# Kernel tuning notes

Measured on AMD Instinct MI355X. Metric: run time of the kernel, lower is better.

The kernel has to match this reference:

```python
import jax, jax.numpy as jnp
import numpy as np

N_NODES = 100000
N_EDGES = 3200000
D_FEAT = 64


def setup_inputs() -> dict:
    key = jax.random.key(0)
    k_x, k_r, k_c, k_v = jax.random.split(key, 4)
    x = jax.random.normal(k_x, (N_NODES, D_FEAT), dtype=jnp.float32)
    edge_row = jax.random.randint(k_r, (N_EDGES,), 0, N_NODES, dtype=jnp.int64)
    edge_col = jax.random.randint(k_c, (N_EDGES,), 0, N_NODES, dtype=jnp.int64)
    # positive values mimicking symmetric-normalized adjacency weights
    edge_val = jax.random.uniform(k_v, (N_EDGES,), dtype=jnp.float32)
    t = jnp.zeros((1,), dtype=jnp.float32)  # ODE time, unused by this linear GCN step
    return {"t": t, "x": x, "edge_row": edge_row, "edge_col": edge_col, "edge_val": edge_val}


def reference(t, x, edge_row, edge_col, edge_val):
    # out = A_sparse @ x, COO SpMM as gather -> scale -> segment-sum scatter
    # gathered: [n_edges, d]
    gathered = edge_val[:, None] * x[edge_col]
    out = jax.ops.segment_sum(gathered, edge_row, num_segments=N_NODES)
    return out
```

## Files before the change

kernel.cpp:

```cpp
#include <hip/hip_runtime.h>
#include <hip/hip_bf16.h>
#include <hip/hip_fp16.h>

#define D 64
#define RB 128
#define NB_MAX 1024
#define NBLK1 512
#define P1CAP 6272
#define CAP 5120

typedef unsigned long long ull;
typedef unsigned short u16;

__device__ __forceinline__ ull pack_rec(float v, int r, int c) {
    return ((ull)__float_as_uint(v) << 32) |
           (ull)(((unsigned)(r & (RB - 1)) << 17) | (unsigned)c);
}

__global__ __launch_bounds__(256) void spmm_atomic_kernel(
    const float* __restrict__ x,
    const int*   __restrict__ edge_row,
    const int*   __restrict__ edge_col,
    const float* __restrict__ edge_val,
    float*       __restrict__ out,
    int n_edges)
{
    const int gtid = blockIdx.x * blockDim.x + threadIdx.x;
    const int wave = gtid >> 6;
    const int lane = threadIdx.x & 63;
    if (wave >= n_edges) return;
    const int   r = edge_row[wave];
    const int   c = edge_col[wave];
    const float v = edge_val[wave];
    atomicAdd(&out[(size_t)r * D + lane], v * x[(size_t)c * D + lane]);
}

__global__ __launch_bounds__(256) void p1a_hist_kernel(
    const int* __restrict__ rows, u16* __restrict__ counts,
    int n_edges, int nb, int chunk)
{
    __shared__ int cnt[NB_MAX];
    const int t = threadIdx.x, blk = blockIdx.x;
    const int e0 = blk * chunk;
    const int e1 = min(e0 + chunk, n_edges);

    for (int i = t; i < nb; i += 256) cnt[i] = 0;
    __syncthreads();
    for (int i = e0 + t * 4; i < e1; i += 1024) {
        if (i + 4 <= e1) {
            const int4 r4 = *(const int4*)(rows + i);
            atomicAdd(&cnt[r4.x >> 7], 1);
            atomicAdd(&cnt[r4.y >> 7], 1);
            atomicAdd(&cnt[r4.z >> 7], 1);
            atomicAdd(&cnt[r4.w >> 7], 1);
        } else {
            for (int k = i; k < e1; ++k) atomicAdd(&cnt[rows[k] >> 7], 1);
        }
    }
    __syncthreads();
    for (int i = t; i < nb; i += 256)
        counts[(size_t)i * NBLK1 + blk] = (u16)cnt[i];
}

__global__ __launch_bounds__(256) void p2_scanblocks_kernel(
    const u16* __restrict__ counts, int* __restrict__ dest32,
    int* __restrict__ binsum, int nb)
{
    __shared__ int s[256];
    const int b = blockIdx.x, t = threadIdx.x;
    const int la = (int)counts[(size_t)b * NBLK1 + 2 * t];
    const int lb = (int)counts[(size_t)b * NBLK1 + 2 * t + 1];
    const int mysum = la + lb;
    s[t] = mysum;
    for (int off = 1; off < 256; off <<= 1) {
        __syncthreads();
        const int w = (t >= off) ? s[t - off] : 0;
        __syncthreads();
        s[t] += w;
    }
    const int excl = s[t] - mysum;
    dest32[(size_t)b * NBLK1 + 2 * t]     = excl;
    dest32[(size_t)b * NBLK1 + 2 * t + 1] = excl + la;
    if (t == 255) binsum[b] = s[255];
}

__global__ __launch_bounds__(1024) void p3_scanbins_kernel(
    const int* __restrict__ binsum, int* __restrict__ binbase,
    int* __restrict__ flags, int nb)
{
    __shared__ int s[1024];
    const int t = threadIdx.x;
    const int mine = (t < nb) ? binsum[t] : 0;
    s[t] = mine;
    for (int off = 1; off < 1024; off <<= 1) {
        __syncthreads();
        const int v = (t >= off) ? s[t - off] : 0;
        __syncthreads();
        s[t] += v;
    }
    if (t < nb) { binbase[t] = s[t] - mine; flags[t] = 0; }
    if (t == nb - 1) binbase[nb] = s[t];
}

__global__ __launch_bounds__(256) void p1b_sortwrite_kernel(
    const int* __restrict__ rows, const int* __restrict__ cols,
    const float* __restrict__ vals,
    const u16* __restrict__ counts, const int* __restrict__ dest32,
    const int* __restrict__ binbase,
    ull* __restrict__ recs, int n_edges, int nb, int chunk)
{
    __shared__ ull stage[P1CAP];
    __shared__ u16 binof[P1CAP];
    __shared__ int cnt[NB_MAX];
    __shared__ u16 doffL[NB_MAX];
    __shared__ int gbase[NB_MAX];
    __shared__ int s[256];
    const int t = threadIdx.x, blk = blockIdx.x;
    const int e0 = blk * chunk;
    const int e1 = min(e0 + chunk, n_edges);
    const int len = e1 - e0;

    int pre[4], sum = 0, c4[4];
    const int base = t * 4;
    #pragma unroll
    for (int k = 0; k < 4; ++k) {
        const int idx = base + k;
        c4[k] = (idx < nb) ? (int)counts[(size_t)idx * NBLK1 + blk] : 0;
        pre[k] = sum; sum += c4[k];
    }
    s[t] = sum;
    for (int off = 1; off < 256; off <<= 1) {
        __syncthreads();
        const int w = (t >= off) ? s[t - off] : 0;
        __syncthreads();
        s[t] += w;
    }
    const int texcl = s[t] - sum;
    __syncthreads();
    #pragma unroll
    for (int k = 0; k < 4; ++k) {
        const int idx = base + k;
        if (idx < nb) {
            const int e = texcl + pre[k];
            cnt[idx]   = e;
            doffL[idx] = (u16)e;
            gbase[idx] = binbase[idx] + dest32[(size_t)idx * NBLK1 + blk];
        }
    }
    __syncthreads();

    for (int i = e0 + t * 4; i < e1; i += 1024) {
        if (i + 4 <= e1) {
            const int4   r4  = *(const int4*)(rows + i);
            const int4   c4v = *(const int4*)(cols + i);
            const float4 v4  = *(const float4*)(vals + i);
            int p;
            p = atomicAdd(&cnt[r4.x >> 7], 1); stage[p] = pack_rec(v4.x, r4.x, c4v.x); binof[p] = (u16)(r4.x >> 7);
            p = atomicAdd(&cnt[r4.y >> 7], 1); stage[p] = pack_rec(v4.y, r4.y, c4v.y); binof[p] = (u16)(r4.y >> 7);
            p = atomicAdd(&cnt[r4.z >> 7], 1); stage[p] = pack_rec(v4.z, r4.z, c4v.z); binof[p] = (u16)(r4.z >> 7);
            p = atomicAdd(&cnt[r4.w >> 7], 1); stage[p] = pack_rec(v4.w, r4.w, c4v.w); binof[p] = (u16)(r4.w >> 7);
        } else {
            for (int k = i; k < e1; ++k) {
                const int p = atomicAdd(&cnt[rows[k] >> 7], 1);
                stage[p] = pack_rec(vals[k], rows[k], cols[k]);
                binof[p] = (u16)(rows[k] >> 7);
            }
        }
    }
    __syncthreads();

    for (int i = t; i < len; i += 256) {
        const int bin = (int)binof[i];
        recs[gbase[bin] + (i - (int)doffL[bin])] = stage[i];
    }
}

__global__ __launch_bounds__(256) void p4_sortbin_kernel(
    const int* __restrict__ binbase,
    ull* __restrict__ recs, int* __restrict__ offsets_row, int* __restrict__ flags,
    int n_nodes)
{
    __shared__ ull stage[CAP];
    __shared__ int cnt[1024];
    __shared__ int s[256];
    const int b = blockIdx.x, t = threadIdx.x;
    const int s0  = binbase[b];
    const int len = binbase[b + 1] - s0;

    if (len > CAP) {
        if (t == 0) {
            flags[b] = 1;
            if (b * RB <= n_nodes) offsets_row[b * RB] = s0;
        }
        return;
    }

    for (int i = t; i < 1024; i += 256) cnt[i] = 0;
    __syncthreads();

    for (int i = t; i < len; i += 256) {
        const ull rr = recs[s0 + i];
        stage[i] = rr;
        const int key = ((int)((rr >> 17) & (RB - 1)) << 3) |
                        (int)(((unsigned)rr & 0x1FFFF) >> 14);
        atomicAdd(&cnt[key], 1);
    }
    __syncthreads();

    int v[4], pre[4], sum = 0;
    const int base = t * 4;
    #pragma unroll
    for (int k = 0; k < 4; ++k) { v[k] = cnt[base + k]; pre[k] = sum; sum += v[k]; }
    s[t] = sum;
    for (int off = 1; off < 256; off <<= 1) {
        __syncthreads();
        const int w = (t >= off) ? s[t - off] : 0;
        __syncthreads();
        s[t] += w;
    }
    const int texcl = s[t] - sum;
    __syncthreads();
    #pragma unroll
    for (int k = 0; k < 4; ++k) cnt[base + k] = texcl + pre[k];
    __syncthreads();

    if (t <= RB) {
        const int r = b * RB + t;
        if (r <= n_nodes)
            offsets_row[r] = s0 + ((t == RB) ? len : cnt[t << 3]);
    }
    __syncthreads();

    for (int i = t; i < len; i += 256) {
        const ull rr = stage[i];
        const int key = ((int)((rr >> 17) & (RB - 1)) << 3) |
                        (int)(((unsigned)rr & 0x1FFFF) >> 14);
        const int p = atomicAdd(&cnt[key], 1);
        recs[s0 + p] = rr;
    }
}

__global__ void tohalf_kernel(const float* __restrict__ x,
                              __half2* __restrict__ xh2, int n4)
{
    for (int i = blockIdx.x * blockDim.x + threadIdx.x; i < n4;
         i += gridDim.x * blockDim.x) {
        const float4 v = ((const float4*)x)[i];
        xh2[2 * i + 0] = __floats2half2_rn(v.x, v.y);
        xh2[2 * i + 1] = __floats2half2_rn(v.z, v.w);
    }
}

__global__ __launch_bounds__(256, 8) void spmm_csr_half2_kernel(
    const __half* __restrict__ xh,
    const int*   __restrict__ offsets_row,
    const int*   __restrict__ binbase,
    const ull*   __restrict__ recs,
    const int*   __restrict__ flags,
    float*       __restrict__ out,
    int row_base, int row_end)
{
    const int row  = row_base + blockIdx.x * 4 + (threadIdx.x >> 6);
    if (row >= row_end) return;
    const int lane = threadIdx.x & 63;
    const int b    = row >> 7;

    if (__builtin_expect(flags[b], 0)) {
        float acc = 0.f;
        const int s  = binbase[b];
        const int e  = binbase[b + 1];
        const int lr = row & (RB - 1);
        for (int j = s; j < e; ++j) {
            const ull rec = recs[j];
            if ((int)((rec >> 17) & (RB - 1)) == lr) {
                const int   c = (int)((unsigned)rec & 0x1FFFF);
                const float v = __uint_as_float((unsigned)(rec >> 32));
                acc += v * __half2float(xh[(size_t)c * D + lane]);
            }
        }
        out[(size_t)row * D + lane] = acc;
        return;
    }

    const __half2* xh2 = (const __half2*)xh;
    const int half = lane >> 5;
    const int fl   = lane & 31;

    const int s = offsets_row[row];
    const int e = offsets_row[row + 1];
    float accx = 0.f, accy = 0.f;

    int j = s;
    for (; j + 16 <= e; j += 16) {
        float vv[8]; int aa[8];
        #pragma unroll
        for (int k = 0; k < 8; ++k) {
            const ull rec = recs[j + 2 * k + half];
            vv[k] = __uint_as_float((unsigned)(rec >> 32));
            aa[k] = ((int)((unsigned)rec & 0x1FFFF) << 5) + fl;
        }
        __half2 hv[8];
        #pragma unroll
        for (int k = 0; k < 8; ++k) hv[k] = xh2[aa[k]];
        __builtin_amdgcn_sched_barrier(0);
        #pragma unroll
        for (int k = 0; k < 8; ++k) {
            const float2 xf = __half22float2(hv[k]);
            accx = fmaf(vv[k], xf.x, accx);
            accy = fmaf(vv[k], xf.y, accy);
        }
    }
    if (j < e) {
        const int safe = e - 1;
        float vv[8]; int aa[8];
        #pragma unroll
        for (int k = 0; k < 8; ++k) {
            const int  idx = j + 2 * k + half;
            const bool ok  = idx < e;
            const ull  rec = recs[ok ? idx : safe];
            vv[k] = ok ? __uint_as_float((unsigned)(rec >> 32)) : 0.f;
            aa[k] = ((int)((unsigned)rec & 0x1FFFF) << 5) + fl;
        }
        __half2 hv[8];
        #pragma unroll
        for (int k = 0; k < 8; ++k) hv[k] = xh2[aa[k]];
        __builtin_amdgcn_sched_barrier(0);
        #pragma unroll
        for (int k = 0; k < 8; ++k) {
            const float2 xf = __half22float2(hv[k]);
            accx = fmaf(vv[k], xf.x, accx);
            accy = fmaf(vv[k], xf.y, accy);
        }
    }

    accx += __shfl_xor(accx, 32);
    accy += __shfl_xor(accy, 32);
    if (half == 0) {
        float2 o; o.x = accx; o.y = accy;
        ((float2*)out)[(size_t)row * 32 + fl] = o;
    }
}

static inline size_t align16(size_t v) { return (v + 15) & ~(size_t)15; }

extern "C" void kernel_launch(void* const* d_in, const int* in_sizes, int n_in,
                              void* d_out, int out_size, void* d_ws, size_t ws_size,
                              hipStream_t stream)
{
    const float* x        = (const float*)d_in[1];
    const int*   edge_row = (const int*)d_in[2];
    const int*   edge_col = (const int*)d_in[3];
    const float* edge_val = (const float*)d_in[4];
    float*       out      = (float*)d_out;

    const int n_edges = in_sizes[2];
    const int n_nodes = out_size / D;
    const int nb      = (n_nodes + RB - 1) / RB;
    const int chunk   = (((n_edges + NBLK1 - 1) / NBLK1) + 3) & ~3;

    const size_t off_recs    = 0;
    const size_t off_xh      = align16(off_recs + (size_t)n_edges * 8);
    const size_t off_counts  = align16(off_xh + (size_t)n_nodes * D * 2);
    const size_t off_dest    = align16(off_counts + (size_t)nb * NBLK1 * 2);
    const size_t off_binsum  = align16(off_dest + (size_t)nb * NBLK1 * 4);
    const size_t off_binbase = align16(off_binsum + (size_t)nb * 4);
    const size_t off_rowoffs = align16(off_binbase + (size_t)(nb + 1) * 4);
    const size_t off_flags   = align16(off_rowoffs + (size_t)(n_nodes + 1) * 4);
    const size_t ws_needed   = off_flags + (size_t)nb * 4;

    if (ws_size < ws_needed || nb > NB_MAX || n_nodes > (1 << 17) ||
        chunk > P1CAP || n_edges < 1) {
        hipMemsetAsync(out, 0, (size_t)out_size * sizeof(float), stream);
        const int n_blocks = (n_edges + 3) / 4;
        spmm_atomic_kernel<<<n_blocks, 256, 0, stream>>>(
            x, edge_row, edge_col, edge_val, out, n_edges);
        return;
    }

    char* ws = (char*)d_ws;
    ull*     recs        = (ull*)(ws + off_recs);
    __half*  xh          = (__half*)(ws + off_xh);
    __half2* xh2         = (__half2*)xh;
    u16*     counts      = (u16*)(ws + off_counts);
    int*     dest32      = (int*)(ws + off_dest);
    int*     binsum      = (int*)(ws + off_binsum);
    int*     binbase     = (int*)(ws + off_binbase);
    int*     offsets_row = (int*)(ws + off_rowoffs);
    int*     flags       = (int*)(ws + off_flags);

    const int n4 = (n_nodes * D) / 4;

    p1a_hist_kernel<<<NBLK1, 256, 0, stream>>>(
        edge_row, counts, n_edges, nb, chunk);
    p2_scanblocks_kernel<<<nb, 256, 0, stream>>>(counts, dest32, binsum, nb);
    p3_scanbins_kernel<<<1, 1024, 0, stream>>>(binsum, binbase, flags, nb);
    p1b_sortwrite_kernel<<<NBLK1, 256, 0, stream>>>(
        edge_row, edge_col, edge_val, counts, dest32, binbase,
        recs, n_edges, nb, chunk);
    p4_sortbin_kernel<<<nb, 256, 0, stream>>>(
        binbase, recs, offsets_row, flags, n_nodes);
    tohalf_kernel<<<2048, 256, 0, stream>>>(x, xh2, n4);

    const int third = (((n_nodes + 2) / 3) + 3) & ~3;
    for (int p = 0; p < 3; ++p) {
        const int rb = p * third;
        const int re = min(rb + third, n_nodes);
        if (re > rb) {
            const int grid = (re - rb + 3) / 4;
            spmm_csr_half2_kernel<<<grid, 256, 0, stream>>>(
                xh, offsets_row, binbase, recs, flags, out, rb, re);
        }
    }
}
```

Baseline: 258.8 us.

## Double partition blocks, merge SpMM launches, fold bin offset math

Doubles the number of edge-partition blocks (1024) and halves per-block staging capacity, adapting the per-bin block scan to handle four counts per thread. The scatter write now uses one precomputed global-minus-local offset per bin instead of two lookups. The three row-range SpMM launches are merged into a single launch covering all nodes, removing launch overhead. More blocks should improve occupancy in the sort phases, but they also increase the size of the counts/dest arrays and the scan work.

```diff
diff --git a/kernel.cpp b/kernel.cpp
--- a/kernel.cpp
+++ b/kernel.cpp
@@ -5,8 +5,8 @@
 #define D 64
 #define RB 128
 #define NB_MAX 1024
-#define NBLK1 512
-#define P1CAP 6272
+#define NBLK1 1024
+#define P1CAP 3200
 #define CAP 5120
 
 typedef unsigned long long ull;
@@ -68,19 +68,24 @@
 {
     __shared__ int s[256];
     const int b = blockIdx.x, t = threadIdx.x;
-    const int la = (int)counts[(size_t)b * NBLK1 + 2 * t];
-    const int lb = (int)counts[(size_t)b * NBLK1 + 2 * t + 1];
-    const int mysum = la + lb;
-    s[t] = mysum;
+    const int base = t * 4;
+    int c4[4], pre[4], sum = 0;
+    #pragma unroll
+    for (int k = 0; k < 4; ++k) {
+        c4[k] = (int)counts[(size_t)b * NBLK1 + base + k];
+        pre[k] = sum; sum += c4[k];
+    }
+    s[t] = sum;
     for (int off = 1; off < 256; off <<= 1) {
         __syncthreads();
         const int w = (t >= off) ? s[t - off] : 0;
         __syncthreads();
         s[t] += w;
     }
-    const int excl = s[t] - mysum;
-    dest32[(size_t)b * NBLK1 + 2 * t]     = excl;
-    dest32[(size_t)b * NBLK1 + 2 * t + 1] = excl + la;
+    const int excl = s[t] - sum;
+    #pragma unroll
+    for (int k = 0; k < 4; ++k)
+        dest32[(size_t)b * NBLK1 + base + k] = excl + pre[k];
     if (t == 255) binsum[b] = s[255];
 }
 
@@ -112,8 +117,7 @@
     __shared__ ull stage[P1CAP];
     __shared__ u16 binof[P1CAP];
     __shared__ int cnt[NB_MAX];
-    __shared__ u16 doffL[NB_MAX];
-    __shared__ int gbase[NB_MAX];
+    __shared__ int gmd[NB_MAX];
     __shared__ int s[256];
     const int t = threadIdx.x, blk = blockIdx.x;
     const int e0 = blk * chunk;
@@ -142,9 +146,8 @@
         const int idx = base + k;
         if (idx < nb) {
             const int e = texcl + pre[k];
-            cnt[idx]   = e;
-            doffL[idx] = (u16)e;
-            gbase[idx] = binbase[idx] + dest32[(size_t)idx * NBLK1 + blk];
+            cnt[idx] = e;
+            gmd[idx] = binbase[idx] + dest32[(size_t)idx * NBLK1 + blk] - e;
         }
     }
     __syncthreads();
@@ -169,10 +172,8 @@
     }
     __syncthreads();
 
-    for (int i = t; i < len; i += 256) {
-        const int bin = (int)binof[i];
-        recs[gbase[bin] + (i - (int)doffL[bin])] = stage[i];
-    }
+    for (int i = t; i < len; i += 256)
+        recs[gmd[(int)binof[i]] + i] = stage[i];
 }
 
 __global__ __launch_bounds__(256) void p4_sortbin_kernel(
@@ -258,10 +259,10 @@
     const ull*   __restrict__ recs,
     const int*   __restrict__ flags,
     float*       __restrict__ out,
-    int row_base, int row_end)
-{
-    const int row  = row_base + blockIdx.x * 4 + (threadIdx.x >> 6);
-    if (row >= row_end) return;
+    int n_nodes)
+{
+    const int row  = blockIdx.x * 4 + (threadIdx.x >> 6);
+    if (row >= n_nodes) return;
     const int lane = threadIdx.x & 63;
     const int b    = row >> 7;
 
@@ -401,14 +402,6 @@
         binbase, recs, offsets_row, flags, n_nodes);
     tohalf_kernel<<<2048, 256, 0, stream>>>(x, xh2, n4);
 
-    const int third = (((n_nodes + 2) / 3) + 3) & ~3;
-    for (int p = 0; p < 3; ++p) {
-        const int rb = p * third;
-        const int re = min(rb + third, n_nodes);
-        if (re > rb) {
-            const int grid = (re - rb + 3) / 4;
-            spmm_csr_half2_kernel<<<grid, 256, 0, stream>>>(
-                xh, offsets_row, binbase, recs, flags, out, rb, re);
-        }
-    }
-}
+    spmm_csr_half2_kernel<<<(n_nodes + 3) / 4, 256, 0, stream>>>(
+        xh, offsets_row, binbase, recs, flags, out, n_nodes);
+}
```

After: 258.2 us. Within noise of the previous version (-0.2%).
